# Optimization experiments

Measured on AMD Instinct MI355X. Metric: run time of the kernel, lower is better.

Reference implementation:

```python
import jax, jax.numpy as jnp
import numpy as np

N = 50000      # nodes
E = 800000     # raw edges (self-loops added inside reference, PyG GATConv default)
H = 8          # attention heads
DH = 16        # head dim
HID = H * DH   # 128 hidden
L = 4          # num GAT layers
G = 16         # graphs in the batch
EPS = 1e-5
NEG_SLOPE = 0.2


def setup_inputs() -> dict:
    key = jax.random.key(0)
    ks = jax.random.split(key, 8)
    s = 0.05
    x = jax.random.normal(ks[0], (N, 64), jnp.float32)
    edge_index = jax.random.randint(ks[1], (2, E), 0, N, dtype=jnp.int32).astype(jnp.int64)
    batch = jnp.sort(jax.random.randint(ks[2], (N,), 0, G, dtype=jnp.int32)).astype(jnp.int64)
    in_W = jax.random.normal(ks[3], (64, HID), jnp.float32) * s
    in_b = jnp.zeros((HID,), jnp.float32)
    Wg = jax.random.normal(ks[4], (L, HID, HID), jnp.float32) * s
    att_src = jax.random.normal(ks[5], (L, H, DH), jnp.float32) * s
    att_dst = jax.random.normal(ks[6], (L, H, DH), jnp.float32) * s
    gat_b = jnp.zeros((L, HID), jnp.float32)
    gn_w = jnp.ones((L, HID), jnp.float32)
    gn_b = jnp.zeros((L, HID), jnp.float32)
    gn_s = jnp.ones((L, HID), jnp.float32)  # GraphNorm mean_scale
    return {"x": x, "edge_index": edge_index, "batch": batch, "in_W": in_W,
            "in_b": in_b, "Wg": Wg, "att_src": att_src, "att_dst": att_dst,
            "gat_b": gat_b, "gn_w": gn_w, "gn_b": gn_b, "gn_s": gn_s}


def _gat_conv(h_in, src, dst, W, a_src, a_dst, bias):
    # PyG GATConv: per-head linear, additive attention, softmax over incoming edges
    h = (h_in @ W).reshape(N, H, DH)                       # [N,H,DH]
    e_src = jnp.sum(h * a_src, axis=-1)                    # [N,H]
    e_dst = jnp.sum(h * a_dst, axis=-1)                    # [N,H]
    e = jax.nn.leaky_relu(e_src[src] + e_dst[dst], NEG_SLOPE)  # [E',H]
    m = jax.ops.segment_max(e, dst, num_segments=N)        # per-dst max (stable softmax)
    m = jnp.where(jnp.isfinite(m), m, 0.0)
    ex = jnp.exp(e - m[dst])
    denom = jax.ops.segment_sum(ex, dst, num_segments=N)
    alpha = ex / (denom[dst] + 1e-16)                      # [E',H]
    msg = h[src] * alpha[..., None]                        # [E',H,DH]
    out = jax.ops.segment_sum(msg, dst, num_segments=N)    # [N,H,DH]
    return out.reshape(N, HID) + bias


def _graph_norm(x, batch, w, b, scale):
    cnt = jax.ops.segment_sum(jnp.ones((N, 1), x.dtype), batch, num_segments=G)
    mean = jax.ops.segment_sum(x, batch, num_segments=G) / cnt        # [G,HID]
    out = x - scale * mean[batch]
    var = jax.ops.segment_sum(out * out, batch, num_segments=G) / cnt # [G,HID]
    return out / jnp.sqrt(var + EPS)[batch] * w + b


def reference(x, edge_index, batch, in_W, in_b, Wg, att_src, att_dst, gat_b, gn_w, gn_b, gn_s):
    # add self-loops (PyG GATConv default add_self_loops=True)
    loop = jnp.arange(N, dtype=edge_index.dtype)
    src = jnp.concatenate([edge_index[0], loop])
    dst = jnp.concatenate([edge_index[1], loop])
    h = x @ in_W + in_b                                    # input_proj -> [N,HID]
    for i in range(L):
        attn = _gat_conv(h, src, dst, Wg[i], att_src[i], att_dst[i], gat_b[i])
        h = attn + h                                       # identity residual (in==out)
        h = _graph_norm(h, batch, gn_w[i], gn_b[i], gn_s[i])
        # dropout is identity in eval mode
    return h
```

## Files before the change

kernel.cpp:

```cpp
#include <hip/hip_runtime.h>
#include <cstdint>
#include <cstddef>

#define Nn   50000
#define Ee   800000
#define ETOT 850000
#define HID  128
#define Gg   16
#define RSZ  6250
#define DMAX 64
#define NEG_SLOPE 0.2f
#define EPS_GN 1e-5f

typedef __attribute__((ext_vector_type(8))) short short8;
typedef __attribute__((ext_vector_type(4))) float f32x4;

static __device__ __forceinline__ float lrelu(float v) { return v > 0.f ? v : NEG_SLOPE * v; }

static __device__ __forceinline__ unsigned int f2bf(float x) {
    unsigned int u = __float_as_uint(x);
    return (u + 0x7fffu + ((u >> 16) & 1u)) >> 16;
}
static __device__ __forceinline__ float bf_lo(unsigned int u) { return __uint_as_float(u << 16); }
static __device__ __forceinline__ float bf_hi(unsigned int u) { return __uint_as_float(u & 0xffff0000u); }

__global__ void prep_w(const float* __restrict__ in_W, const float* __restrict__ Wg,
                       short* __restrict__ Wt0, short* __restrict__ Wtl) {
    int i = blockIdx.x * 256 + threadIdx.x;
    if (i < 8192) {
        int n = i >> 6, k = i & 63;
        Wt0[i] = (short)f2bf(in_W[k * 128 + n]);
    } else if (i < 73728) {
        int j = i - 8192;
        int l = j >> 14;
        int rkn = j & 16383;
        int n = rkn >> 7, k = rkn & 127;
        Wtl[j] = (short)f2bf(Wg[l * 16384 + k * 128 + n]);
    }
}

__global__ void scatter_pad(const int* __restrict__ esrc, const int* __restrict__ edst,
                            int* __restrict__ cnt, int* __restrict__ colPad) {
    int r  = blockIdx.x & 7;
    int cb = blockIdx.x >> 3;
    int nb = gridDim.x >> 3;
    int lo = r * RSZ, hi = lo + RSZ;
    for (int i = cb * 256 + threadIdx.x; i < ETOT; i += nb * 256) {
        int dst = (i < Ee) ? edst[i] : (i - Ee);
        if (dst >= lo && dst < hi) {
            int src = (i < Ee) ? esrc[i] : dst;
            int pos = atomicAdd(&cnt[dst], 1);
            if (pos < DMAX) colPad[dst * DMAX + pos] = src;
        }
    }
}

template <int K, bool ABF16, bool AFFINE, bool BIAS, bool SCORES>
__global__ __launch_bounds__(256) void gemm_mfma(const float* __restrict__ Agf,
                                                 const unsigned int* __restrict__ Agb,
                                                 const int* __restrict__ batch,
                                                 const float* __restrict__ Ab,
                                                 const float* __restrict__ Bb,
                                                 const short* __restrict__ Wt,
                                                 const float* __restrict__ bias,
                                                 const float* __restrict__ asrc,
                                                 const float* __restrict__ adst,
                                                 float* __restrict__ es,
                                                 float* __restrict__ ed,
                                                 unsigned int* __restrict__ Cb,
                                                 int M) {
    constexpr int KP = K + 8;
    constexpr int ABYTES = 128 * KP * 2;
    constexpr int CBYTES = 64 * 130 * 4;
    constexpr int SBYTES = ABYTES > CBYTES ? ABYTES : CBYTES;
    __shared__ __align__(16) char smem[SBYTES];
    short* As = (short*)smem;
    float* Cs = (float*)smem;

    int t    = threadIdx.x;
    int lane = t & 63;
    int w    = t >> 6;
    int wm   = (w & 1) * 64;
    int wn   = (w >> 1) * 64;
    int row0 = blockIdx.x * 128;

    if (!ABF16) {
        constexpr int F4R = K / 4;
        constexpr int ITERS = 128 * F4R / 256;
#pragma unroll
        for (int i = 0; i < ITERS; i++) {
            int f4 = t + 256 * i;
            int r  = f4 / F4R;
            int c4 = f4 % F4R;
            float4 v = make_float4(0.f, 0.f, 0.f, 0.f);
            int gr = row0 + r;
            if (gr < M) v = *(const float4*)(Agf + (size_t)gr * K + c4 * 4);
            uint2 pk;
            pk.x = f2bf(v.x) | (f2bf(v.y) << 16);
            pk.y = f2bf(v.z) | (f2bf(v.w) << 16);
            *(uint2*)(As + r * KP + c4 * 4) = pk;
        }
    } else {
        constexpr int U2R = K / 4;
        constexpr int ITERS = 128 * U2R / 256;
#pragma unroll
        for (int i = 0; i < ITERS; i++) {
            int u2 = t + 256 * i;
            int r  = u2 / U2R;
            int c2 = u2 % U2R;
            uint2 v = make_uint2(0u, 0u);
            int gr = row0 + r;
            if (gr < M) {
                v = *(const uint2*)(Agb + (size_t)gr * (K / 2) + c2 * 2);
                if (AFFINE) {
                    int g = batch[gr];
                    float4 Av = *(const float4*)(Ab + g * 128 + c2 * 4);
                    float4 Bv = *(const float4*)(Bb + g * 128 + c2 * 4);
                    float x0 = bf_lo(v.x) * Av.x + Bv.x;
                    float x1 = bf_hi(v.x) * Av.y + Bv.y;
                    float x2 = bf_lo(v.y) * Av.z + Bv.z;
                    float x3 = bf_hi(v.y) * Av.w + Bv.w;
                    v.x = f2bf(x0) | (f2bf(x1) << 16);
                    v.y = f2bf(x2) | (f2bf(x3) << 16);
                }
            }
            *(uint2*)(As + r * KP + c2 * 4) = v;
        }
    }
    __syncthreads();

    f32x4 acc[4][4] = {};
    int am = wm + (lane & 15);
    int aq = (lane >> 4) * 8;
    const short* wb = Wt + (size_t)(wn + (lane & 15)) * K + aq;
#pragma unroll
    for (int kk = 0; kk < K / 32; kk++) {
        short8 a[4], b[4];
#pragma unroll
        for (int nt = 0; nt < 4; nt++)
            b[nt] = *(const short8*)(wb + nt * 16 * K + kk * 32);
#pragma unroll
        for (int mt = 0; mt < 4; mt++)
            a[mt] = *(const short8*)(As + (am + mt * 16) * KP + kk * 32 + aq);
#pragma unroll
        for (int mt = 0; mt < 4; mt++)
#pragma unroll
            for (int nt = 0; nt < 4; nt++)
                acc[mt][nt] = __builtin_amdgcn_mfma_f32_16x16x32_bf16(
                    a[mt], b[nt], acc[mt][nt], 0, 0, 0);
    }

    float bv[4] = {0.f, 0.f, 0.f, 0.f};
    if (BIAS) {
#pragma unroll
        for (int nt = 0; nt < 4; nt++) bv[nt] = bias[wn + nt * 16 + (lane & 15)];
    }
    float avv[8], dvv[8];
    if (SCORES) {
        int q = t & 15;
#pragma unroll
        for (int k = 0; k < 8; k++) {
            avv[k] = asrc[q * 8 + k];
            dvv[k] = adst[q * 8 + k];
        }
    }
#pragma unroll
    for (int half = 0; half < 2; half++) {
        __syncthreads();
        if ((w & 1) == half) {
#pragma unroll
            for (int mt = 0; mt < 4; mt++)
#pragma unroll
                for (int reg = 0; reg < 4; reg++) {
                    int lr = mt * 16 + (lane >> 4) * 4 + reg;
#pragma unroll
                    for (int nt = 0; nt < 4; nt++)
                        Cs[lr * 130 + wn + nt * 16 + (lane & 15)] =
                            acc[mt][nt][reg] + bv[nt];
                }
        }
        __syncthreads();
#pragma unroll
        for (int i = 0; i < 4; i++) {
            int u4 = t + 256 * i;
            int r  = u4 >> 4;
            int cu = (u4 & 15) * 4;
            int grow = row0 + half * 64 + r;
            if (grow < M) {
                const float* cp = Cs + r * 130 + cu * 2;
                float2 p0 = *(const float2*)(cp + 0);
                float2 p1 = *(const float2*)(cp + 2);
                float2 p2 = *(const float2*)(cp + 4);
                float2 p3 = *(const float2*)(cp + 6);
                uint4 o;
                o.x = f2bf(p0.x) | (f2bf(p0.y) << 16);
                o.y = f2bf(p1.x) | (f2bf(p1.y) << 16);
                o.z = f2bf(p2.x) | (f2bf(p2.y) << 16);
                o.w = f2bf(p3.x) | (f2bf(p3.y) << 16);
                *(uint4*)(Cb + (size_t)grow * 64 + cu) = o;
                if (SCORES) {
                    float s1 = p0.x * avv[0] + p0.y * avv[1] + p1.x * avv[2] +
                               p1.y * avv[3] + p2.x * avv[4] + p2.y * avv[5] +
                               p3.x * avv[6] + p3.y * avv[7];
                    float s2 = p0.x * dvv[0] + p0.y * dvv[1] + p1.x * dvv[2] +
                               p1.y * dvv[3] + p2.x * dvv[4] + p2.y * dvv[5] +
                               p3.x * dvv[6] + p3.y * dvv[7];
                    s1 += __shfl_xor(s1, 1);
                    s2 += __shfl_xor(s2, 1);
                    if ((t & 1) == 0) {
                        int hh = (t & 15) >> 1;
                        es[(size_t)grow * 8 + hh] = s1;
                        ed[(size_t)grow * 8 + hh] = s2;
                    }
                }
            }
        }
    }
}

template <bool AFF>
__global__ __launch_bounds__(256) void gat_attn(const unsigned int* __restrict__ hp,
                                                const unsigned int* hinb,
                                                const int* __restrict__ batch,
                                                const float* __restrict__ Ab,
                                                const float* __restrict__ Bb,
                                                const float* __restrict__ es,
                                                const float* __restrict__ ed,
                                                const int* __restrict__ cnt,
                                                const int* __restrict__ colPad,
                                                const float* __restrict__ gbias,
                                                unsigned int* outb) {
    int w    = threadIdx.x >> 6;
    int lane = threadIdx.x & 63;
    int n    = blockIdx.x * 4 + w;
    int deg  = cnt[n];
    deg = deg < DMAX ? deg : DMAX;
    const int* cb = colPad + n * DMAX;

    int slot = lane >> 3;
    int ah   = lane & 7;
    int half = lane >> 5;
    int sl   = lane & 31;
    int hd   = sl >> 2;

    float edh = ed[(size_t)n * 8 + ah];
    const unsigned int* hpl = hp + sl * 2;

    float a0 = 0.f, a1 = 0.f, a2 = 0.f, a3 = 0.f;
    float dacc = 0.f;

    int e0 = 0;
    for (; e0 + 8 <= deg; e0 += 8) {
        int src_l = cb[e0 + slot];
        float wgt = __expf(lrelu(es[(size_t)src_l * 8 + ah] + edh));
        dacc += wgt;
#pragma unroll
        for (int jj = 0; jj < 4; jj++) {
            int e = jj * 2 + half;
            int   sj = __shfl(src_l, e * 8);
            float wj = __shfl(wgt,   e * 8 + hd);
            uint2 hv = *(const uint2*)(hpl + (size_t)sj * 64);
            a0 += wj * bf_lo(hv.x);
            a1 += wj * bf_hi(hv.x);
            a2 += wj * bf_lo(hv.y);
            a3 += wj * bf_hi(hv.y);
        }
    }
    if (e0 < deg) {
        int rem = deg - e0;
        int ee  = e0 + slot;
        int ec  = (slot < rem) ? ee : (deg - 1);
        int src_l = cb[ec];
        float wgt = (slot < rem) ? __expf(lrelu(es[(size_t)src_l * 8 + ah] + edh)) : 0.f;
        dacc += wgt;
        int steps = (rem + 1) >> 1;
        for (int jj = 0; jj < steps; jj++) {
            int e = jj * 2 + half;
            int   sj = __shfl(src_l, e * 8);
            float wj = __shfl(wgt,   e * 8 + hd);
            uint2 hv = *(const uint2*)(hpl + (size_t)sj * 64);
            a0 += wj * bf_lo(hv.x);
            a1 += wj * bf_hi(hv.x);
            a2 += wj * bf_lo(hv.y);
            a3 += wj * bf_hi(hv.y);
        }
    }

    a0 += __shfl_xor(a0, 32);
    a1 += __shfl_xor(a1, 32);
    a2 += __shfl_xor(a2, 32);
    a3 += __shfl_xor(a3, 32);

    dacc += __shfl_xor(dacc, 8);
    dacc += __shfl_xor(dacc, 16);
    dacc += __shfl_xor(dacc, 32);
    float inv  = 1.0f / (dacc + 1e-16f);
    float winv = __shfl(inv, hd);

    if (half == 0) {
        size_t uo = (size_t)n * 64 + sl * 2;
        uint2 xv = *(const uint2*)(hinb + uo);
        float r0 = bf_lo(xv.x), r1 = bf_hi(xv.x), r2 = bf_lo(xv.y), r3 = bf_hi(xv.y);
        if (AFF) {
            int g = batch[n];
            float4 Av = *(const float4*)(Ab + g * 128 + sl * 4);
            float4 Bv = *(const float4*)(Bb + g * 128 + sl * 4);
            r0 = r0 * Av.x + Bv.x;
            r1 = r1 * Av.y + Bv.y;
            r2 = r2 * Av.z + Bv.z;
            r3 = r3 * Av.w + Bv.w;
        }
        float4 bv = *(const float4*)(gbias + sl * 4);
        float o0 = a0 * winv + bv.x + r0;
        float o1 = a1 * winv + bv.y + r1;
        float o2 = a2 * winv + bv.z + r2;
        float o3 = a3 * winv + bv.w + r3;
        uint2 o;
        o.x = f2bf(o0) | (f2bf(o1) << 16);
        o.y = f2bf(o2) | (f2bf(o3) << 16);
        *(uint2*)(outb + uo) = o;
    }
}

#define SCHUNK 64
__global__ __launch_bounds__(128) void gn_stats(const unsigned int* __restrict__ xb,
                                                const int* __restrict__ batch,
                                                float* __restrict__ sumx,
                                                float* __restrict__ sumxx,
                                                float* __restrict__ cnt) {
    int c  = threadIdx.x;
    int cu = c >> 1;
    int hi = c & 1;
    int n0 = blockIdx.x * SCHUNK;
    int n1 = n0 + SCHUNK;
    if (n1 > Nn) n1 = Nn;
    if (n0 >= Nn) return;
    int curG = batch[n0];
    float sx = 0.f, sxx = 0.f;
    int run = 0;
    for (int n = n0; n < n1; n++) {
        int g = batch[n];
        if (g != curG) {
            atomicAdd(&sumx[curG * 128 + c], sx);
            atomicAdd(&sumxx[curG * 128 + c], sxx);
            if (c == 0) atomicAdd(&cnt[curG], (float)run);
            sx = 0.f; sxx = 0.f; run = 0; curG = g;
        }
        unsigned int u = xb[(size_t)n * 64 + cu];
        float v = hi ? bf_hi(u) : bf_lo(u);
        sx += v; sxx += v * v; run++;
    }
    atomicAdd(&sumx[curG * 128 + c], sx);
    atomicAdd(&sumxx[curG * 128 + c], sxx);
    if (c == 0) atomicAdd(&cnt[curG], (float)run);
}

__global__ void gn_final(float* __restrict__ sumx, float* __restrict__ sumxx,
                         float* __restrict__ cnt, const float* __restrict__ w,
                         const float* __restrict__ b, const float* __restrict__ s,
                         float* __restrict__ Ab, float* __restrict__ Bb) {
    int i = blockIdx.x * blockDim.x + threadIdx.x;
    if (i >= Gg * 128) return;
    int g = i >> 7, c = i & 127;
    float cn  = cnt[g];
    float m   = sumx[i] / cn;
    float msq = sumxx[i] / cn;
    float sc  = s[c];
    float varo = msq - (2.f * sc - sc * sc) * m * m;
    float inv  = rsqrtf(varo + EPS_GN);
    float Ai   = inv * w[c];
    Ab[i] = Ai;
    Bb[i] = b[c] - sc * m * Ai;
    __syncthreads();
    sumx[i] = 0.f;
    sumxx[i] = 0.f;
    if (c == 0) cnt[g] = 0.f;
}

__global__ __launch_bounds__(256) void gn_apply(const unsigned int* __restrict__ xb,
                                                const int* __restrict__ batch,
                                                const float* __restrict__ Ab,
                                                const float* __restrict__ Bb,
                                                float* __restrict__ out) {
    int idx = blockIdx.x * 256 + threadIdx.x;
    int n = idx >> 5;
    if (n >= Nn) return;
    int c4 = (idx & 31) << 2;
    int g = batch[n];
    uint2 xv = *(const uint2*)(xb + (size_t)n * 64 + (c4 >> 1));
    float4 Av = *(const float4*)(Ab + g * 128 + c4);
    float4 Bv = *(const float4*)(Bb + g * 128 + c4);
    float4 o;
    o.x = bf_lo(xv.x) * Av.x + Bv.x;
    o.y = bf_hi(xv.x) * Av.y + Bv.y;
    o.z = bf_lo(xv.y) * Av.z + Bv.z;
    o.w = bf_hi(xv.y) * Av.w + Bv.w;
    *(float4*)(out + (size_t)n * 128 + c4) = o;
}

extern "C" void kernel_launch(void* const* d_in, const int* in_sizes, int n_in,
                              void* d_out, int out_size, void* d_ws, size_t ws_size,
                              hipStream_t stream) {
    const float* x      = (const float*)d_in[0];
    const int*   eidx   = (const int*)d_in[1];
    const int*   batch  = (const int*)d_in[2];
    const float* in_W   = (const float*)d_in[3];
    const float* in_b   = (const float*)d_in[4];
    const float* Wg     = (const float*)d_in[5];
    const float* attS   = (const float*)d_in[6];
    const float* attD   = (const float*)d_in[7];
    const float* gat_b  = (const float*)d_in[8];
    const float* gn_w   = (const float*)d_in[9];
    const float* gn_b   = (const float*)d_in[10];
    const float* gn_s   = (const float*)d_in[11];

    const int* esrc = eidx;
    const int* edst = eidx + Ee;

    char* p = (char*)d_ws;
    auto carve = [&](size_t bytes) {
        void* r = (void*)p;
        p += (bytes + 255) & ~(size_t)255;
        return r;
    };
    unsigned int* h0b = (unsigned int*)carve((size_t)Nn * 64 * 4);
    unsigned int* hp  = (unsigned int*)carve((size_t)Nn * 64 * 4);
    unsigned int* h2b = (unsigned int*)carve((size_t)Nn * 64 * 4);
    float* es   = (float*)carve((size_t)Nn * 8 * 4);
    float* ed   = (float*)carve((size_t)Nn * 8 * 4);
    int*   cnt  = (int*)carve((size_t)(Nn + Gg * 128 * 2 + 16) * 4);
    float* sumx  = (float*)(cnt + Nn);
    float* sumxx = sumx + Gg * 128;
    float* cntf  = sumx + Gg * 128 * 2;
    float* Abuf = (float*)carve((size_t)Gg * 128 * 4);
    float* Bbuf = (float*)carve((size_t)Gg * 128 * 4);
    int* colPad = (int*)carve((size_t)Nn * DMAX * 4);
    short* Wt0  = (short*)carve((size_t)128 * 64 * 2);
    short* Wtl  = (short*)carve((size_t)4 * 128 * 128 * 2);

    prep_w<<<288, 256, 0, stream>>>(in_W, Wg, Wt0, Wtl);
    hipMemsetAsync(cnt, 0, (size_t)(Nn + Gg * 128 * 2 + 16) * 4, stream);
    scatter_pad<<<768, 256, 0, stream>>>(esrc, edst, cnt, colPad);

    const int gemm_grid = (Nn + 127) / 128;

    gemm_mfma<64, false, false, true, false><<<gemm_grid, 256, 0, stream>>>(
        x, nullptr, nullptr, nullptr, nullptr, Wt0, in_b,
        nullptr, nullptr, nullptr, nullptr, h0b, Nn);

    for (int l = 0; l < 4; l++) {
        const short* Wl = Wtl + (size_t)l * 128 * 128;
        if (l == 0) {
            gemm_mfma<128, true, false, false, true><<<gemm_grid, 256, 0, stream>>>(
                nullptr, h0b, nullptr, nullptr, nullptr, Wl, nullptr,
                attS + l * 128, attD + l * 128, es, ed, hp, Nn);
            gat_attn<false><<<Nn / 4, 256, 0, stream>>>(hp, h0b, nullptr, nullptr, nullptr,
                                                        es, ed, cnt, colPad,
                                                        gat_b + l * 128, h2b);
        } else {
            gemm_mfma<128, true, true, false, true><<<gemm_grid, 256, 0, stream>>>(
                nullptr, h2b, batch, Abuf, Bbuf, Wl, nullptr,
                attS + l * 128, attD + l * 128, es, ed, hp, Nn);
            gat_attn<true><<<Nn / 4, 256, 0, stream>>>(hp, h2b, batch, Abuf, Bbuf,
                                                       es, ed, cnt, colPad,
                                                       gat_b + l * 128, h2b);
        }
        gn_stats<<<(Nn + SCHUNK - 1) / SCHUNK, 128, 0, stream>>>(h2b, batch, sumx, sumxx, cntf);
        gn_final<<<8, 256, 0, stream>>>(sumx, sumxx, cntf, gn_w + l * 128,
                                        gn_b + l * 128, gn_s + l * 128, Abuf, Bbuf);
    }
    gn_apply<<<(Nn * 32 + 255) / 256, 256, 0, stream>>>(h2b, batch, Abuf, Bbuf,
                                                        (float*)d_out);
    (void)in_sizes; (void)n_in; (void)out_size; (void)ws_size;
}
```

Baseline: 507.8 us.

## Fuse GraphNorm stats into attention kernel and compute affine on the fly

Removes the separate gn_stats and gn_final kernels per layer. GraphNorm sums and sums of squares are now accumulated inside gat_attn with block-level shared atomics, and the per-graph node counts are computed once in prep_w. Consumers (the GEMM, the attention residual, gn_apply) derive the scale and shift on the fly from the raw stats. The attention block grows to 1024 threads (16 nodes) and the scatter grid is enlarged. This saves launches and one full pass over h per layer, at the cost of more global atomics and some redundant recomputation of the affine terms.

```diff
diff --git a/kernel.cpp b/kernel.cpp
--- a/kernel.cpp
+++ b/kernel.cpp
@@ -24,8 +24,21 @@
 static __device__ __forceinline__ float bf_lo(unsigned int u) { return __uint_as_float(u << 16); }
 static __device__ __forceinline__ float bf_hi(unsigned int u) { return __uint_as_float(u & 0xffff0000u); }
 
+static __device__ __forceinline__ void gn_ab(float sx, float sq, float cn,
+                                             float wv, float bv, float sv,
+                                             float& A, float& B) {
+    float m    = sx / cn;
+    float msq  = sq / cn;
+    float varo = msq - (2.f * sv - sv * sv) * m * m;
+    float inv  = rsqrtf(varo + EPS_GN);
+    A = inv * wv;
+    B = bv - sv * m * A;
+}
+
 __global__ void prep_w(const float* __restrict__ in_W, const float* __restrict__ Wg,
-                       short* __restrict__ Wt0, short* __restrict__ Wtl) {
+                       const int* __restrict__ batch,
+                       short* __restrict__ Wt0, short* __restrict__ Wtl,
+                       float* __restrict__ cntf) {
     int i = blockIdx.x * 256 + threadIdx.x;
     if (i < 8192) {
         int n = i >> 6, k = i & 63;
@@ -36,6 +49,16 @@
         int rkn = j & 16383;
         int n = rkn >> 7, k = rkn & 127;
         Wtl[j] = (short)f2bf(Wg[l * 16384 + k * 128 + n]);
+    } else if (i < 73728 + 6250) {
+        int base = (i - 73728) * 8;
+        int g = batch[base];
+        float c = 1.f;
+        for (int k = 1; k < 8; k++) {
+            int gk = batch[base + k];
+            if (gk != g) { atomicAdd(&cntf[g], c); g = gk; c = 1.f; }
+            else c += 1.f;
+        }
+        atomicAdd(&cntf[g], c);
     }
 }
 
@@ -59,8 +82,12 @@
 __global__ __launch_bounds__(256) void gemm_mfma(const float* __restrict__ Agf,
                                                  const unsigned int* __restrict__ Agb,
                                                  const int* __restrict__ batch,
-                                                 const float* __restrict__ Ab,
-                                                 const float* __restrict__ Bb,
+                                                 const float* __restrict__ sxP,
+                                                 const float* __restrict__ sqP,
+                                                 const float* __restrict__ cntf,
+                                                 const float* __restrict__ gw,
+                                                 const float* __restrict__ gb,
+                                                 const float* __restrict__ gs,
                                                  const short* __restrict__ Wt,
                                                  const float* __restrict__ bias,
                                                  const float* __restrict__ asrc,
@@ -74,6 +101,7 @@
     constexpr int CBYTES = 64 * 130 * 4;
     constexpr int SBYTES = ABYTES > CBYTES ? ABYTES : CBYTES;
     __shared__ __align__(16) char smem[SBYTES];
+    __shared__ float AffA[2][132], AffB[2][132];
     short* As = (short*)smem;
     float* Cs = (float*)smem;
 
@@ -83,6 +111,21 @@
     int wm   = (w & 1) * 64;
     int wn   = (w >> 1) * 64;
     int row0 = blockIdx.x * 128;
+
+    int g0 = 0, g1 = 0;
+    if (AFFINE) {
+        g0 = batch[row0];
+        int lastr = row0 + 127 < M - 1 ? row0 + 127 : M - 1;
+        g1 = batch[lastr];
+        int sel = t >> 7;
+        int c   = t & 127;
+        int g   = sel ? g1 : g0;
+        float A, B;
+        gn_ab(sxP[g * 128 + c], sqP[g * 128 + c], cntf[g], gw[c], gb[c], gs[c], A, B);
+        AffA[sel][c] = A;
+        AffB[sel][c] = B;
+        __syncthreads();
+    }
 
     if (!ABF16) {
         constexpr int F4R = K / 4;
@@ -113,9 +156,9 @@
             if (gr < M) {
                 v = *(const uint2*)(Agb + (size_t)gr * (K / 2) + c2 * 2);
                 if (AFFINE) {
-                    int g = batch[gr];
-                    float4 Av = *(const float4*)(Ab + g * 128 + c2 * 4);
-                    float4 Bv = *(const float4*)(Bb + g * 128 + c2 * 4);
+                    int sel = (batch[gr] == g0) ? 0 : 1;
+                    float4 Av = *(const float4*)(&AffA[sel][c2 * 4]);
+                    float4 Bv = *(const float4*)(&AffB[sel][c2 * 4]);
                     float x0 = bf_lo(v.x) * Av.x + Bv.x;
                     float x1 = bf_hi(v.x) * Av.y + Bv.y;
                     float x2 = bf_lo(v.y) * Av.z + Bv.z;
@@ -219,23 +262,31 @@
 }
 
 template <bool AFF>
-__global__ __launch_bounds__(256) void gat_attn(const unsigned int* __restrict__ hp,
-                                                const unsigned int* hinb,
-                                                const int* __restrict__ batch,
-                                                const float* __restrict__ Ab,
-                                                const float* __restrict__ Bb,
-                                                const float* __restrict__ es,
-                                                const float* __restrict__ ed,
-                                                const int* __restrict__ cnt,
-                                                const int* __restrict__ colPad,
-                                                const float* __restrict__ gbias,
-                                                unsigned int* outb) {
-    int w    = threadIdx.x >> 6;
-    int lane = threadIdx.x & 63;
-    int n    = blockIdx.x * 4 + w;
+__global__ __launch_bounds__(1024) void gat_attn(const unsigned int* __restrict__ hp,
+                                                 const unsigned int* hinb,
+                                                 const int* __restrict__ batch,
+                                                 const float* __restrict__ sxP,
+                                                 const float* __restrict__ sqP,
+                                                 const float* __restrict__ cntf,
+                                                 const float* __restrict__ gw,
+                                                 const float* __restrict__ gb,
+                                                 const float* __restrict__ gs,
+                                                 const float* __restrict__ es,
+                                                 const float* __restrict__ ed,
+                                                 const int* __restrict__ cnt,
+                                                 const int* __restrict__ colPad,
+                                                 const float* __restrict__ gbias,
+                                                 unsigned int* outb,
+                                                 float* __restrict__ sxO,
+                                                 float* __restrict__ sqO) {
+    __shared__ float s_sum[128], s_sq[128];
+    int t    = threadIdx.x;
+    int w    = t >> 6;
+    int lane = t & 63;
+    int n    = blockIdx.x * 16 + w;
     int deg  = cnt[n];
     deg = deg < DMAX ? deg : DMAX;
-    const int* cb = colPad + n * DMAX;
+    const int* cbp = colPad + n * DMAX;
 
     int slot = lane >> 3;
     int ah   = lane & 7;
@@ -251,7 +302,7 @@
 
     int e0 = 0;
     for (; e0 + 8 <= deg; e0 += 8) {
-        int src_l = cb[e0 + slot];
+        int src_l = cbp[e0 + slot];
         float wgt = __expf(lrelu(es[(size_t)src_l * 8 + ah] + edh));
         dacc += wgt;
 #pragma unroll
@@ -270,7 +321,7 @@
         int rem = deg - e0;
         int ee  = e0 + slot;
         int ec  = (slot < rem) ? ee : (deg - 1);
-        int src_l = cb[ec];
+        int src_l = cbp[ec];
         float wgt = (slot < rem) ? __expf(lrelu(es[(size_t)src_l * 8 + ah] + edh)) : 0.f;
         dacc += wgt;
         int steps = (rem + 1) >> 1;
@@ -297,104 +348,89 @@
     float inv  = 1.0f / (dacc + 1e-16f);
     float winv = __shfl(inv, hd);
 
+    float o0 = 0.f, o1 = 0.f, o2 = 0.f, o3 = 0.f;
     if (half == 0) {
         size_t uo = (size_t)n * 64 + sl * 2;
         uint2 xv = *(const uint2*)(hinb + uo);
         float r0 = bf_lo(xv.x), r1 = bf_hi(xv.x), r2 = bf_lo(xv.y), r3 = bf_hi(xv.y);
         if (AFF) {
             int g = batch[n];
-            float4 Av = *(const float4*)(Ab + g * 128 + sl * 4);
-            float4 Bv = *(const float4*)(Bb + g * 128 + sl * 4);
-            r0 = r0 * Av.x + Bv.x;
-            r1 = r1 * Av.y + Bv.y;
-            r2 = r2 * Av.z + Bv.z;
-            r3 = r3 * Av.w + Bv.w;
+            float cn = cntf[g];
+            int c = sl * 4;
+            float A, B;
+            gn_ab(sxP[g * 128 + c],     sqP[g * 128 + c],     cn, gw[c],     gb[c],     gs[c],     A, B);
+            r0 = r0 * A + B;
+            gn_ab(sxP[g * 128 + c + 1], sqP[g * 128 + c + 1], cn, gw[c + 1], gb[c + 1], gs[c + 1], A, B);
+            r1 = r1 * A + B;
+            gn_ab(sxP[g * 128 + c + 2], sqP[g * 128 + c + 2], cn, gw[c + 2], gb[c + 2], gs[c + 2], A, B);
+            r2 = r2 * A + B;
+            gn_ab(sxP[g * 128 + c + 3], sqP[g * 128 + c + 3], cn, gw[c + 3], gb[c + 3], gs[c + 3], A, B);
+            r3 = r3 * A + B;
         }
         float4 bv = *(const float4*)(gbias + sl * 4);
-        float o0 = a0 * winv + bv.x + r0;
-        float o1 = a1 * winv + bv.y + r1;
-        float o2 = a2 * winv + bv.z + r2;
-        float o3 = a3 * winv + bv.w + r3;
+        o0 = a0 * winv + bv.x + r0;
+        o1 = a1 * winv + bv.y + r1;
+        o2 = a2 * winv + bv.z + r2;
+        o3 = a3 * winv + bv.w + r3;
         uint2 o;
         o.x = f2bf(o0) | (f2bf(o1) << 16);
         o.y = f2bf(o2) | (f2bf(o3) << 16);
         *(uint2*)(outb + uo) = o;
     }
-}
-
-#define SCHUNK 64
-__global__ __launch_bounds__(128) void gn_stats(const unsigned int* __restrict__ xb,
-                                                const int* __restrict__ batch,
-                                                float* __restrict__ sumx,
-                                                float* __restrict__ sumxx,
-                                                float* __restrict__ cnt) {
-    int c  = threadIdx.x;
-    int cu = c >> 1;
-    int hi = c & 1;
-    int n0 = blockIdx.x * SCHUNK;
-    int n1 = n0 + SCHUNK;
-    if (n1 > Nn) n1 = Nn;
-    if (n0 >= Nn) return;
-    int curG = batch[n0];
-    float sx = 0.f, sxx = 0.f;
-    int run = 0;
-    for (int n = n0; n < n1; n++) {
-        int g = batch[n];
-        if (g != curG) {
-            atomicAdd(&sumx[curG * 128 + c], sx);
-            atomicAdd(&sumxx[curG * 128 + c], sxx);
-            if (c == 0) atomicAdd(&cnt[curG], (float)run);
-            sx = 0.f; sxx = 0.f; run = 0; curG = g;
-        }
-        unsigned int u = xb[(size_t)n * 64 + cu];
-        float v = hi ? bf_hi(u) : bf_lo(u);
-        sx += v; sxx += v * v; run++;
-    }
-    atomicAdd(&sumx[curG * 128 + c], sx);
-    atomicAdd(&sumxx[curG * 128 + c], sxx);
-    if (c == 0) atomicAdd(&cnt[curG], (float)run);
-}
-
-__global__ void gn_final(float* __restrict__ sumx, float* __restrict__ sumxx,
-                         float* __restrict__ cnt, const float* __restrict__ w,
-                         const float* __restrict__ b, const float* __restrict__ s,
-                         float* __restrict__ Ab, float* __restrict__ Bb) {
-    int i = blockIdx.x * blockDim.x + threadIdx.x;
-    if (i >= Gg * 128) return;
-    int g = i >> 7, c = i & 127;
-    float cn  = cnt[g];
-    float m   = sumx[i] / cn;
-    float msq = sumxx[i] / cn;
-    float sc  = s[c];
-    float varo = msq - (2.f * sc - sc * sc) * m * m;
-    float inv  = rsqrtf(varo + EPS_GN);
-    float Ai   = inv * w[c];
-    Ab[i] = Ai;
-    Bb[i] = b[c] - sc * m * Ai;
-    __syncthreads();
-    sumx[i] = 0.f;
-    sumxx[i] = 0.f;
-    if (c == 0) cnt[g] = 0.f;
+
+    int g0b = batch[blockIdx.x * 16];
+    int g1b = batch[blockIdx.x * 16 + 15];
+    if (g0b == g1b) {
+        if (t < 128) { s_sum[t] = 0.f; s_sq[t] = 0.f; }
+        __syncthreads();
+        if (half == 0) {
+            int c = sl * 4;
+            atomicAdd(&s_sum[c],     o0); atomicAdd(&s_sq[c],     o0 * o0);
+            atomicAdd(&s_sum[c + 1], o1); atomicAdd(&s_sq[c + 1], o1 * o1);
+            atomicAdd(&s_sum[c + 2], o2); atomicAdd(&s_sq[c + 2], o2 * o2);
+            atomicAdd(&s_sum[c + 3], o3); atomicAdd(&s_sq[c + 3], o3 * o3);
+        }
+        __syncthreads();
+        if (t < 128)       atomicAdd(&sxO[g0b * 128 + t], s_sum[t]);
+        else if (t < 256)  atomicAdd(&sqO[g0b * 128 + (t - 128)], s_sq[t - 128]);
+    } else {
+        if (half == 0) {
+            int g = batch[n];
+            int c = sl * 4;
+            atomicAdd(&sxO[g * 128 + c],     o0); atomicAdd(&sqO[g * 128 + c],     o0 * o0);
+            atomicAdd(&sxO[g * 128 + c + 1], o1); atomicAdd(&sqO[g * 128 + c + 1], o1 * o1);
+            atomicAdd(&sxO[g * 128 + c + 2], o2); atomicAdd(&sqO[g * 128 + c + 2], o2 * o2);
+            atomicAdd(&sxO[g * 128 + c + 3], o3); atomicAdd(&sqO[g * 128 + c + 3], o3 * o3);
+        }
+    }
 }
 
 __global__ __launch_bounds__(256) void gn_apply(const unsigned int* __restrict__ xb,
                                                 const int* __restrict__ batch,
-                                                const float* __restrict__ Ab,
-                                                const float* __restrict__ Bb,
+                                                const float* __restrict__ sx,
+                                                const float* __restrict__ sq,
+                                                const float* __restrict__ cntf,
+                                                const float* __restrict__ gw,
+                                                const float* __restrict__ gb,
+                                                const float* __restrict__ gs,
                                                 float* __restrict__ out) {
     int idx = blockIdx.x * 256 + threadIdx.x;
     int n = idx >> 5;
     if (n >= Nn) return;
     int c4 = (idx & 31) << 2;
     int g = batch[n];
+    float cn = cntf[g];
     uint2 xv = *(const uint2*)(xb + (size_t)n * 64 + (c4 >> 1));
-    float4 Av = *(const float4*)(Ab + g * 128 + c4);
-    float4 Bv = *(const float4*)(Bb + g * 128 + c4);
+    float vv[4] = {bf_lo(xv.x), bf_hi(xv.x), bf_lo(xv.y), bf_hi(xv.y)};
     float4 o;
-    o.x = bf_lo(xv.x) * Av.x + Bv.x;
-    o.y = bf_hi(xv.x) * Av.y + Bv.y;
-    o.z = bf_lo(xv.y) * Av.z + Bv.z;
-    o.w = bf_hi(xv.y) * Av.w + Bv.w;
+    float* op = (float*)&o;
+#pragma unroll
+    for (int k = 0; k < 4; k++) {
+        int c = c4 + k;
+        float A, B;
+        gn_ab(sx[g * 128 + c], sq[g * 128 + c], cn, gw[c], gb[c], gs[c], A, B);
+        op[k] = vv[k] * A + B;
+    }
     *(float4*)(out + (size_t)n * 128 + c4) = o;
 }
 
@@ -428,48 +464,50 @@
     unsigned int* h2b = (unsigned int*)carve((size_t)Nn * 64 * 4);
     float* es   = (float*)carve((size_t)Nn * 8 * 4);
     float* ed   = (float*)carve((size_t)Nn * 8 * 4);
-    int*   cnt  = (int*)carve((size_t)(Nn + Gg * 128 * 2 + 16) * 4);
-    float* sumx  = (float*)(cnt + Nn);
-    float* sumxx = sumx + Gg * 128;
-    float* cntf  = sumx + Gg * 128 * 2;
-    float* Abuf = (float*)carve((size_t)Gg * 128 * 4);
-    float* Bbuf = (float*)carve((size_t)Gg * 128 * 4);
+    const size_t ZN = (size_t)Nn + 16 + 4 * 4096;
+    int*   cnt  = (int*)carve(ZN * 4);
+    float* cntf = (float*)(cnt + Nn);
+    float* stats = cntf + 16;
     int* colPad = (int*)carve((size_t)Nn * DMAX * 4);
     short* Wt0  = (short*)carve((size_t)128 * 64 * 2);
     short* Wtl  = (short*)carve((size_t)4 * 128 * 128 * 2);
 
-    prep_w<<<288, 256, 0, stream>>>(in_W, Wg, Wt0, Wtl);
-    hipMemsetAsync(cnt, 0, (size_t)(Nn + Gg * 128 * 2 + 16) * 4, stream);
-    scatter_pad<<<768, 256, 0, stream>>>(esrc, edst, cnt, colPad);
+    hipMemsetAsync(cnt, 0, ZN * 4, stream);
+    prep_w<<<313, 256, 0, stream>>>(in_W, Wg, batch, Wt0, Wtl, cntf);
+    scatter_pad<<<3072, 256, 0, stream>>>(esrc, edst, cnt, colPad);
 
     const int gemm_grid = (Nn + 127) / 128;
 
     gemm_mfma<64, false, false, true, false><<<gemm_grid, 256, 0, stream>>>(
-        x, nullptr, nullptr, nullptr, nullptr, Wt0, in_b,
-        nullptr, nullptr, nullptr, nullptr, h0b, Nn);
+        x, nullptr, nullptr, nullptr, nullptr, nullptr, nullptr, nullptr, nullptr,
+        Wt0, in_b, nullptr, nullptr, nullptr, nullptr, h0b, Nn);
 
     for (int l = 0; l < 4; l++) {
         const short* Wl = Wtl + (size_t)l * 128 * 128;
+        float* sxO = stats + (size_t)l * 4096;
+        float* sqO = sxO + 2048;
         if (l == 0) {
             gemm_mfma<128, true, false, false, true><<<gemm_grid, 256, 0, stream>>>(
-                nullptr, h0b, nullptr, nullptr, nullptr, Wl, nullptr,
-                attS + l * 128, attD + l * 128, es, ed, hp, Nn);
-            gat_attn<false><<<Nn / 4, 256, 0, stream>>>(hp, h0b, nullptr, nullptr, nullptr,
-                                                        es, ed, cnt, colPad,
-                                                        gat_b + l * 128, h2b);
+                nullptr, h0b, nullptr, nullptr, nullptr, nullptr, nullptr, nullptr, nullptr,
+                Wl, nullptr, attS, attD, es, ed, hp, Nn);
+            gat_attn<false><<<Nn / 16, 1024, 0, stream>>>(
+                hp, h0b, batch, nullptr, nullptr, nullptr, nullptr, nullptr, nullptr,
+                es, ed, cnt, colPad, gat_b, h2b, sxO, sqO);
         } else {
+            const float* sxP = stats + (size_t)(l - 1) * 4096;
+            const float* sqP = sxP + 2048;
             gemm_mfma<128, true, true, false, true><<<gemm_grid, 256, 0, stream>>>(
-                nullptr, h2b, batch, Abuf, Bbuf, Wl, nullptr,
-                attS + l * 128, attD + l * 128, es, ed, hp, Nn);
-            gat_attn<true><<<Nn / 4, 256, 0, stream>>>(hp, h2b, batch, Abuf, Bbuf,
-                                                       es, ed, cnt, colPad,
-                                                       gat_b + l * 128, h2b);
-        }
-        gn_stats<<<(Nn + SCHUNK - 1) / SCHUNK, 128, 0, stream>>>(h2b, batch, sumx, sumxx, cntf);
-        gn_final<<<8, 256, 0, stream>>>(sumx, sumxx, cntf, gn_w + l * 128,
-                                        gn_b + l * 128, gn_s + l * 128, Abuf, Bbuf);
-    }
-    gn_apply<<<(Nn * 32 + 255) / 256, 256, 0, stream>>>(h2b, batch, Abuf, Bbuf,
-                                                        (float*)d_out);
+                nullptr, h2b, batch, sxP, sqP, cntf,
+                gn_w + (l - 1) * 128, gn_b + (l - 1) * 128, gn_s + (l - 1) * 128,
+                Wl, nullptr, attS + l * 128, attD + l * 128, es, ed, hp, Nn);
+            gat_attn<true><<<Nn / 16, 1024, 0, stream>>>(
+                hp, h2b, batch, sxP, sqP, cntf,
+                gn_w + (l - 1) * 128, gn_b + (l - 1) * 128, gn_s + (l - 1) * 128,
+                es, ed, cnt, colPad, gat_b + l * 128, h2b, sxO, sqO);
+        }
+    }
+    gn_apply<<<(Nn * 32 + 255) / 256, 256, 0, stream>>>(
+        h2b, batch, stats + 3 * 4096, stats + 3 * 4096 + 2048, cntf,
+        gn_w + 3 * 128, gn_b + 3 * 128, gn_s + 3 * 128, (float*)d_out);
     (void)in_sizes; (void)n_in; (void)out_size; (void)ws_size;
 }
```

Measured after the change: 784.5 us. +54.5%, slower.
